# Performance work log

Measured on AMD Instinct MI355X. Metric: run time of the kernel, lower is better.

The kernel has to match this reference:

```python
import jax, jax.numpy as jnp
import numpy as np

N_NODES = 100000
N_EDGES = 3200000
IN_CH, HID, OUT_CH = 128, 16, 64


def gcn_conv(x, W, b, row, col, n_nodes):
    # PyG GCNConv: add self loops, symmetric deg^{-1/2} normalization,
    # linear transform, scatter-add aggregation at target nodes (col).
    x = x @ W  # [N, out]
    deg = jax.ops.segment_sum(jnp.ones_like(col, dtype=x.dtype), col,
                              num_segments=n_nodes)  # includes self loops
    inv_sqrt = jnp.where(deg > 0, jax.lax.rsqrt(deg), 0.0)
    norm = inv_sqrt[row] * inv_sqrt[col]  # [E+N]
    msgs = x[row] * norm[:, None]  # gather + scale
    out = jax.ops.segment_sum(msgs, col, num_segments=n_nodes)
    return out + b


def setup_inputs() -> dict:
    key = jax.random.key(0)
    ks = jax.random.split(key, 12)
    x = jax.random.normal(ks[0], (N_NODES, IN_CH), dtype=jnp.float32)
    edge_index = jax.random.randint(ks[1], (2, N_EDGES), 0, N_NODES, dtype=jnp.int64)

    def glorot(k, fan_in, fan_out):
        s = jnp.sqrt(6.0 / (fan_in + fan_out))
        return jax.random.uniform(k, (fan_in, fan_out), jnp.float32, -s, s)

    return {
        'x': x,
        'edge_index': edge_index,
        'conv1_W': glorot(ks[2], IN_CH, HID),
        'conv1_b': jnp.zeros((HID,), jnp.float32),
        'conv2_W': glorot(ks[3], HID, OUT_CH),
        'conv2_b': jnp.zeros((OUT_CH,), jnp.float32),
        't1_W': glorot(ks[4], IN_CH, HID),
        't1_b': jnp.zeros((HID,), jnp.float32),
        't2_W': glorot(ks[5], HID, OUT_CH),
        't2_b': jnp.zeros((OUT_CH,), jnp.float32),
    }


def reference(x, edge_index, conv1_W, conv1_b, conv2_W, conv2_b,
              t1_W, t1_b, t2_W, t2_b):
    n = x.shape[0]
    # add self loops once (fixed shape)
    loops = jnp.arange(n, dtype=edge_index.dtype)
    row = jnp.concatenate([edge_index[0], loops])
    col = jnp.concatenate([edge_index[1], loops])

    identity1 = x @ t1_W + t1_b
    h = jax.nn.relu(gcn_conv(x, conv1_W, conv1_b, row, col, n)) + identity1
    identity2 = h @ t2_W + t2_b
    out = jax.nn.relu(gcn_conv(h, conv2_W, conv2_b, row, col, n)) + identity2
    return out
```

## Files before the change

### kernel.cpp

```cpp
#include <hip/hip_runtime.h>

#define INCH 128
#define C1   16
#define C2   64
#define LOCB 7
#define BNODES (1 << LOCB)
#define CAP  8192
#define ROWBITS 17
#define ROWMASK ((1 << ROWBITS) - 1)
#define SENT 0xFFFFFFFFu
#define ACC2P 9
#define FXS   512.0f
#define INVFX 0.001953125f
#define U16B  32768.5f
#define BSH   15
#define BKT_T 1024
#define AGG_T 512

typedef int iv4 __attribute__((ext_vector_type(4)));

__global__ void binit_kernel(int* __restrict__ gcur, int K) {
    int t = blockIdx.x * blockDim.x + threadIdx.x;
    if (t < K) gcur[t] = t * CAP;
}

__global__ __launch_bounds__(BKT_T) void bucket_kernel(
    const int* __restrict__ row, const int* __restrict__ col,
    int* __restrict__ gcur, int* __restrict__ barr,
    int e, int n, int K, int nblocks)
{
    __shared__ int cnt[1024];
    __shared__ int cur[1024];
    __shared__ int sst[1024];
    int tid = threadIdx.x;
    int e4 = e >> 2;
    long b0 = (long)blockIdx.x * e4 / nblocks;
    long b1 = (long)(blockIdx.x + 1) * e4 / nblocks;
    const iv4* c4p = (const iv4*)col;
    const iv4* r4p = (const iv4*)row;
    cnt[tid] = 0;
    __syncthreads();
    for (long i = b0 + tid; i < b1; i += BKT_T) {
        iv4 c4 = c4p[i], r4 = r4p[i];
        #pragma unroll
        for (int k = 0; k < 4; ++k) {
            unsigned c = (unsigned)c4[k], r = (unsigned)r4[k];
            if (c < (unsigned)n && r < (unsigned)n)
                atomicAdd(&cnt[c >> LOCB], 1);
        }
    }
    if (blockIdx.x == 0) {
        for (int i = e4 * 4 + tid; i < e; i += BKT_T) {
            unsigned c = (unsigned)col[i], r = (unsigned)row[i];
            if (c < (unsigned)n && r < (unsigned)n)
                atomicAdd(&cnt[c >> LOCB], 1);
        }
    }
    __syncthreads();
    if (tid < K) {
        int c = cnt[tid];
        int start = c ? atomicAdd(&gcur[tid], (c + 15) & ~15) : 0;
        cur[tid] = start;
        sst[tid] = start;
    }
    __syncthreads();
    for (long i = b0 + tid; i < b1; i += BKT_T) {
        iv4 c4 = c4p[i], r4 = r4p[i];
        #pragma unroll
        for (int k = 0; k < 4; ++k) {
            unsigned c = (unsigned)c4[k], r = (unsigned)r4[k];
            if (c < (unsigned)n && r < (unsigned)n) {
                int b = c >> LOCB;
                int slot = atomicAdd(&cur[b], 1);
                if ((unsigned)slot < (unsigned)((b + 1) * CAP))
                    barr[slot] = (int)(r | ((c & (BNODES - 1)) << ROWBITS));
            }
        }
    }
    if (blockIdx.x == 0) {
        for (int i = e4 * 4 + tid; i < e; i += BKT_T) {
            unsigned c = (unsigned)col[i], r = (unsigned)row[i];
            if (c < (unsigned)n && r < (unsigned)n) {
                int b = c >> LOCB;
                int slot = atomicAdd(&cur[b], 1);
                if ((unsigned)slot < (unsigned)((b + 1) * CAP))
                    barr[slot] = (int)(r | ((c & (BNODES - 1)) << ROWBITS));
            }
        }
    }
    __syncthreads();
    if (tid < K) {
        int c = cnt[tid];
        if (c) {
            int start = sst[tid];
            int end = start + c;
            int re  = start + ((c + 15) & ~15);
            int lim = (tid + 1) * CAP;
            if (end > lim) end = lim;
            if (re  > lim) re  = lim;
            for (int j = end; j < re; ++j) barr[j] = (int)SENT;
        }
    }
}

__global__ __launch_bounds__(AGG_T) void degree_kernel(
    const int* __restrict__ barr, const int* __restrict__ gcur,
    int* __restrict__ deg, int n)
{
    __shared__ int lcnt[BNODES];
    int b = blockIdx.x, tid = threadIdx.x;
    if (tid < BNODES) lcnt[tid] = 0;
    __syncthreads();
    int base = b * CAP;
    int len = gcur[b] - base;
    if (len < 0) len = 0;
    if (len > CAP) len = CAP;
    int len4 = len >> 2;
    const iv4* b4 = (const iv4*)(barr + base);
    for (int i = tid; i < len4; i += AGG_T) {
        iv4 p4 = b4[i];
        #pragma unroll
        for (int k = 0; k < 4; ++k) {
            unsigned pk = (unsigned)p4[k];
            if ((pk & ROWMASK) < (unsigned)n)
                atomicAdd(&lcnt[(pk >> ROWBITS) & (BNODES - 1)], 1);
        }
    }
    __syncthreads();
    if (tid < BNODES) {
        int node = (b << LOCB) + tid;
        if (node < n) deg[node] = lcnt[tid];
    }
}

__device__ __forceinline__ unsigned short enc16(float v) {
    float c = fminf(fmaxf(v, -63.0f), 63.0f);
    return (unsigned short)(c * FXS + U16B);
}

__global__ __launch_bounds__(256) void linear1_kernel(
    const float* __restrict__ x, const float* __restrict__ W1,
    const float* __restrict__ T1, const float* __restrict__ t1b,
    const int* __restrict__ deg,
    unsigned short* __restrict__ xu16, float* __restrict__ xT1, int n)
{
    __shared__ float Wc[INCH][32];
    __shared__ float xs[16][INCH + 4];
    int tid = threadIdx.x;

    for (int i = tid; i < INCH * C1; i += 256) {
        int k = i / C1, c = i % C1;
        Wc[k][c]      = W1[i];
        Wc[k][c + 16] = T1[i];
    }
    int node0 = blockIdx.x * 16;
    for (int i = tid; i < 16 * (INCH / 4); i += 256) {
        int r = i / (INCH / 4);
        int cc = i % (INCH / 4);
        int node = node0 + r;
        float4 v = make_float4(0.f, 0.f, 0.f, 0.f);
        if (node < n) v = ((const float4*)x)[(size_t)node * (INCH / 4) + cc];
        ((float4*)&xs[r][0])[cc] = v;
    }
    __syncthreads();

    int ch = tid & 15, nl = tid >> 4;
    int node = node0 + nl;
    if (node >= n) return;
    float a1 = 0.f, a2 = 0.f;
    #pragma unroll
    for (int k = 0; k < INCH; ++k) {
        float xv = xs[nl][k];
        a1 += xv * Wc[k][ch];
        a2 += xv * Wc[k][ch + 16];
    }
    float ic = rsqrtf((float)(deg[node] + 1));
    xu16[(node << 4) + ch] = enc16(a1 * ic);
    xT1[(node << 4) + ch]  = a2 + t1b[ch];
}

#define EDGE_GS(PK, G)                                                        \
    do {                                                                      \
        if (((PK) & ROWMASK) < un) {                                          \
            unsigned long long* _a = &acc[(((PK) >> ROWBITS) & (BNODES - 1))][tb]; \
            _Pragma("unroll")                                                 \
            for (int _j = 0; _j < 4; ++_j) {                                  \
                unsigned _d = (unsigned)(G)[_j];                              \
                atomicAdd(&_a[_j],                                            \
                    ((unsigned long long)(_d >> 16) << 32) | (_d & 0xFFFFu)); \
            }                                                                 \
        }                                                                     \
    } while (0)

#define GATHER_SCATTER(TBL)                                                   \
    {                                                                         \
        int jj = tid >> 1;                                                    \
        for (int i0 = jj * 4; i0 + 3 < len; i0 += (AGG_T * 2)) {              \
            iv4 w = *(const iv4*)(bp + i0);                                   \
            unsigned s0 = (unsigned)w[0] & ROWMASK, s1 = (unsigned)w[1] & ROWMASK; \
            unsigned s2 = (unsigned)w[2] & ROWMASK, s3 = (unsigned)w[3] & ROWMASK; \
            unsigned c0 = s0 < un ? s0 : 0u, c1 = s1 < un ? s1 : 0u;          \
            unsigned c2 = s2 < un ? s2 : 0u, c3 = s3 < un ? s3 : 0u;          \
            iv4 g0 = *(const iv4*)(TBL + ((size_t)c0 << 3) + tb4);            \
            iv4 g1 = *(const iv4*)(TBL + ((size_t)c1 << 3) + tb4);            \
            iv4 g2 = *(const iv4*)(TBL + ((size_t)c2 << 3) + tb4);            \
            iv4 g3 = *(const iv4*)(TBL + ((size_t)c3 << 3) + tb4);            \
            EDGE_GS((unsigned)w[0], g0);                                      \
            EDGE_GS((unsigned)w[1], g1);                                      \
            EDGE_GS((unsigned)w[2], g2);                                      \
            EDGE_GS((unsigned)w[3], g3);                                      \
        }                                                                     \
    }

__global__ __launch_bounds__(AGG_T) void agg1_bucket_kernel(
    const int* __restrict__ barr, const int* __restrict__ gcur,
    const int* __restrict__ deg, const unsigned short* __restrict__ xu16,
    const float* __restrict__ xT1, const float* __restrict__ b1,
    float* __restrict__ h, unsigned short* __restrict__ hu16, int n)
{
    __shared__ unsigned long long acc[BNODES][ACC2P];
    int b = blockIdx.x, tid = threadIdx.x;
    for (int i = tid; i < BNODES * ACC2P; i += AGG_T) (&acc[0][0])[i] = 0ull;
    __syncthreads();

    int base = b * CAP;
    int len = gcur[b] - base;
    if (len < 0) len = 0;
    if (len > CAP) len = CAP;
    const int* bp = barr + base;
    const unsigned* tblw = (const unsigned*)xu16;
    unsigned un = (unsigned)n;
    int tb4 = (tid & 1) << 2;
    int tb  = (tid & 1) << 2;

    GATHER_SCATTER(tblw)
    __syncthreads();

    const unsigned* au = (const unsigned*)&acc[0][0];
    for (int t = tid; t < BNODES * C1; t += AGG_T) {
        int loc = t >> 4, ch = t & 15;
        int node = (b << LOCB) + loc;
        if (node >= n) continue;
        int idx = (node << 4) + ch;
        int dg = deg[node];
        unsigned wd = au[loc * (2 * ACC2P) + ch];
        int tot = (int)(wd + xu16[idx] - ((unsigned)(dg + 1) << BSH));
        float ic = rsqrtf((float)(dg + 1));
        float v = (float)tot * INVFX * ic + b1[ch];
        float hv = fmaxf(v, 0.f) + xT1[idx];
        h[idx]    = hv;
        hu16[idx] = enc16(hv * ic);
    }
}

__global__ __launch_bounds__(AGG_T) void agg2_bucket_kernel(
    const int* __restrict__ barr, const int* __restrict__ gcur,
    const int* __restrict__ deg, const unsigned short* __restrict__ hu16,
    const float* __restrict__ h,
    const float* __restrict__ W2, const float* __restrict__ T2,
    const float* __restrict__ b2, const float* __restrict__ t2b,
    float* __restrict__ out, int n)
{
    __shared__ unsigned long long acc[BNODES][ACC2P];
    __shared__ float Wc[C1][128];
    __shared__ float h_s[BNODES][C1];
    __shared__ float accf[BNODES][C1 + 1];
    int b = blockIdx.x, tid = threadIdx.x;
    for (int i = tid; i < BNODES * ACC2P; i += AGG_T) (&acc[0][0])[i] = 0ull;
    for (int i = tid; i < C1 * 128; i += AGG_T) {
        int k = i >> 7, c = i & 127;
        Wc[k][c] = (c < 64) ? W2[k * C2 + c] : T2[k * C2 + (c - 64)];
    }
    {
        int node0 = b << LOCB;
        for (int t = tid; t < BNODES * C1 / 4; t += AGG_T) {
            float4 v = make_float4(0.f, 0.f, 0.f, 0.f);
            if (node0 + (t >> 2) < n) v = ((const float4*)h)[(size_t)node0 * 4 + t];
            ((float4*)&h_s[0][0])[t] = v;
        }
    }
    __syncthreads();

    int base = b * CAP;
    int len = gcur[b] - base;
    if (len < 0) len = 0;
    if (len > CAP) len = CAP;
    const int* bp = barr + base;
    const unsigned* tblw = (const unsigned*)hu16;
    unsigned un = (unsigned)n;
    int tb4 = (tid & 1) << 2;
    int tb  = (tid & 1) << 2;

    GATHER_SCATTER(tblw)
    __syncthreads();

    const unsigned* au = (const unsigned*)&acc[0][0];
    for (int t = tid; t < BNODES * C1; t += AGG_T) {
        int loc = t >> 4, ch = t & 15;
        int node = (b << LOCB) + loc;
        float v = 0.f;
        if (node < n) {
            int dg = deg[node];
            unsigned wd = au[loc * (2 * ACC2P) + ch];
            int tot = (int)(wd + hu16[(node << 4) + ch] - ((unsigned)(dg + 1) << BSH));
            v = (float)tot * INVFX * rsqrtf((float)(dg + 1));
        }
        accf[loc][ch] = v;
    }
    __syncthreads();

    int och = tid & 63, g = tid >> 6;
    float w1r[C1], w2r[C1];
    #pragma unroll
    for (int k = 0; k < C1; ++k) { w1r[k] = Wc[k][och]; w2r[k] = Wc[k][och + 64]; }
    float bb = b2[och], tb2 = t2b[och];
    for (int q = 0; q < 16; ++q) {
        int loc = (g << 4) + q;
        int node2 = (b << LOCB) + loc;
        if (node2 >= n) continue;
        float s1 = bb, s2 = tb2;
        #pragma unroll
        for (int k = 0; k < C1; ++k) {
            s1 += accf[loc][k] * w1r[k];
            s2 += h_s[loc][k]  * w2r[k];
        }
        out[(size_t)node2 * C2 + och] = fmaxf(s1, 0.f) + s2;
    }
}

extern "C" void kernel_launch(void* const* d_in, const int* in_sizes, int n_in,
                              void* d_out, int out_size, void* d_ws, size_t ws_size,
                              hipStream_t stream) {
    const float* x   = (const float*)d_in[0];
    const int*   ei  = (const int*)d_in[1];
    const float* W1  = (const float*)d_in[2];
    const float* b1  = (const float*)d_in[3];
    const float* W2  = (const float*)d_in[4];
    const float* b2  = (const float*)d_in[5];
    const float* T1  = (const float*)d_in[6];
    const float* t1b = (const float*)d_in[7];
    const float* T2  = (const float*)d_in[8];
    const float* t2b = (const float*)d_in[9];
    float* out = (float*)d_out;

    const int n = in_sizes[0] / INCH;
    const int e = in_sizes[1] / 2;
    const int* row = ei;
    const int* col = ei + e;
    const int K = (n + BNODES - 1) >> LOCB;

    char* ws = (char*)d_ws;
    int*            gcur = (int*)ws;                  ws += 4096;
    int*            deg  = (int*)ws;                  ws += (size_t)n * 4;
    float*          xT1  = (float*)ws;                ws += (size_t)n * C1 * 4;
    float*          h    = (float*)ws;                ws += (size_t)n * C1 * 4;
    unsigned short* xu16 = (unsigned short*)ws;       ws += (size_t)n * C1 * 2;
    unsigned short* hu16 = (unsigned short*)ws;       ws += (size_t)n * C1 * 2;
    int*            barr = (int*)ws;                  ws += (size_t)K * CAP * 4;

    const int nbb = 390;

    binit_kernel  <<<(K + 255) / 256, 256, 0, stream>>>(gcur, K);
    bucket_kernel <<<nbb, BKT_T, 0, stream>>>(row, col, gcur, barr, e, n, K, nbb);
    degree_kernel <<<K, AGG_T, 0, stream>>>(barr, gcur, deg, n);

    linear1_kernel <<<(n + 15) / 16, 256, 0, stream>>>(x, W1, T1, t1b, deg, xu16, xT1, n);
    agg1_bucket_kernel<<<K, AGG_T, 0, stream>>>(barr, gcur, deg, xu16, xT1, b1, h, hu16, n);
    agg2_bucket_kernel<<<K, AGG_T, 0, stream>>>(barr, gcur, deg, hu16, h,
                                                W2, T2, b2, t2b, out, n);
}
```

Baseline: 250.9 us.

## Raise fixed-point scale, replace bucket init with memset, vectorize linear1 dot

Switches the bucket cursor to relative offsets so the init kernel can be replaced by a hipMemsetAsync, and the aggregation kernels compute the base from the bucket index. The linear1 weights are stored transposed so each thread reads float4 vectors from shared memory with four partial sums, instead of scalar strided reads. Separately, the 16-bit fixed-point encoding is changed to scale 1024 with a clamp at ±31. That gains precision but raises the risk of saturating large activations or overflowing accumulators.

```diff
diff --git a/kernel.cpp b/kernel.cpp
--- a/kernel.cpp
+++ b/kernel.cpp
@@ -10,19 +10,14 @@
 #define ROWMASK ((1 << ROWBITS) - 1)
 #define SENT 0xFFFFFFFFu
 #define ACC2P 9
-#define FXS   512.0f
-#define INVFX 0.001953125f
+#define FXS   1024.0f
+#define INVFX 0.0009765625f
 #define U16B  32768.5f
 #define BSH   15
 #define BKT_T 1024
 #define AGG_T 512
 
 typedef int iv4 __attribute__((ext_vector_type(4)));
-
-__global__ void binit_kernel(int* __restrict__ gcur, int K) {
-    int t = blockIdx.x * blockDim.x + threadIdx.x;
-    if (t < K) gcur[t] = t * CAP;
-}
 
 __global__ __launch_bounds__(BKT_T) void bucket_kernel(
     const int* __restrict__ row, const int* __restrict__ col,
@@ -59,7 +54,8 @@
     __syncthreads();
     if (tid < K) {
         int c = cnt[tid];
-        int start = c ? atomicAdd(&gcur[tid], (c + 15) & ~15) : 0;
+        int rel = c ? atomicAdd(&gcur[tid], (c + 15) & ~15) : 0;
+        int start = tid * CAP + rel;
         cur[tid] = start;
         sst[tid] = start;
     }
@@ -111,12 +107,11 @@
     int b = blockIdx.x, tid = threadIdx.x;
     if (tid < BNODES) lcnt[tid] = 0;
     __syncthreads();
-    int base = b * CAP;
-    int len = gcur[b] - base;
+    int len = gcur[b];
     if (len < 0) len = 0;
     if (len > CAP) len = CAP;
     int len4 = len >> 2;
-    const iv4* b4 = (const iv4*)(barr + base);
+    const iv4* b4 = (const iv4*)(barr + b * CAP);
     for (int i = tid; i < len4; i += AGG_T) {
         iv4 p4 = b4[i];
         #pragma unroll
@@ -134,7 +129,7 @@
 }
 
 __device__ __forceinline__ unsigned short enc16(float v) {
-    float c = fminf(fmaxf(v, -63.0f), 63.0f);
+    float c = fminf(fmaxf(v, -31.0f), 31.0f);
     return (unsigned short)(c * FXS + U16B);
 }
 
@@ -144,19 +139,18 @@
     const int* __restrict__ deg,
     unsigned short* __restrict__ xu16, float* __restrict__ xT1, int n)
 {
-    __shared__ float Wc[INCH][32];
+    __shared__ float WcT[32][INCH + 4];
     __shared__ float xs[16][INCH + 4];
     int tid = threadIdx.x;
 
     for (int i = tid; i < INCH * C1; i += 256) {
-        int k = i / C1, c = i % C1;
-        Wc[k][c]      = W1[i];
-        Wc[k][c + 16] = T1[i];
+        int k = i >> 4, c = i & 15;
+        WcT[c][k]      = W1[i];
+        WcT[c + 16][k] = T1[i];
     }
     int node0 = blockIdx.x * 16;
     for (int i = tid; i < 16 * (INCH / 4); i += 256) {
-        int r = i / (INCH / 4);
-        int cc = i % (INCH / 4);
+        int r = i >> 5, cc = i & 31;
         int node = node0 + r;
         float4 v = make_float4(0.f, 0.f, 0.f, 0.f);
         if (node < n) v = ((const float4*)x)[(size_t)node * (INCH / 4) + cc];
@@ -167,13 +161,23 @@
     int ch = tid & 15, nl = tid >> 4;
     int node = node0 + nl;
     if (node >= n) return;
-    float a1 = 0.f, a2 = 0.f;
+    const float4* xp  = (const float4*)&xs[nl][0];
+    const float4* w1p = (const float4*)&WcT[ch][0];
+    const float4* w2p = (const float4*)&WcT[ch + 16][0];
+    float4 s1 = make_float4(0.f, 0.f, 0.f, 0.f);
+    float4 s2 = make_float4(0.f, 0.f, 0.f, 0.f);
     #pragma unroll
-    for (int k = 0; k < INCH; ++k) {
-        float xv = xs[nl][k];
-        a1 += xv * Wc[k][ch];
-        a2 += xv * Wc[k][ch + 16];
-    }
+    for (int k4 = 0; k4 < INCH / 4; ++k4) {
+        float4 xv = xp[k4];
+        float4 wa = w1p[k4];
+        float4 wb = w2p[k4];
+        s1.x += xv.x * wa.x; s1.y += xv.y * wa.y;
+        s1.z += xv.z * wa.z; s1.w += xv.w * wa.w;
+        s2.x += xv.x * wb.x; s2.y += xv.y * wb.y;
+        s2.z += xv.z * wb.z; s2.w += xv.w * wb.w;
+    }
+    float a1 = (s1.x + s1.y) + (s1.z + s1.w);
+    float a2 = (s2.x + s2.y) + (s2.z + s2.w);
     float ic = rsqrtf((float)(deg[node] + 1));
     xu16[(node << 4) + ch] = enc16(a1 * ic);
     xT1[(node << 4) + ch]  = a2 + t1b[ch];
@@ -223,11 +227,10 @@
     for (int i = tid; i < BNODES * ACC2P; i += AGG_T) (&acc[0][0])[i] = 0ull;
     __syncthreads();
 
-    int base = b * CAP;
-    int len = gcur[b] - base;
+    int len = gcur[b];
     if (len < 0) len = 0;
     if (len > CAP) len = CAP;
-    const int* bp = barr + base;
+    const int* bp = barr + b * CAP;
     const unsigned* tblw = (const unsigned*)xu16;
     unsigned un = (unsigned)n;
     int tb4 = (tid & 1) << 2;
@@ -281,11 +284,10 @@
     }
     __syncthreads();
 
-    int base = b * CAP;
-    int len = gcur[b] - base;
+    int len = gcur[b];
     if (len < 0) len = 0;
     if (len > CAP) len = CAP;
-    const int* bp = barr + base;
+    const int* bp = barr + b * CAP;
     const unsigned* tblw = (const unsigned*)hu16;
     unsigned un = (unsigned)n;
     int tb4 = (tid & 1) << 2;
@@ -360,7 +362,7 @@
 
     const int nbb = 390;
 
-    binit_kernel  <<<(K + 255) / 256, 256, 0, stream>>>(gcur, K);
+    hipMemsetAsync(gcur, 0, 4096, stream);
     bucket_kernel <<<nbb, BKT_T, 0, stream>>>(row, col, gcur, barr, e, n, K, nbb);
     degree_kernel <<<K, AGG_T, 0, stream>>>(barr, gcur, deg, n);
 
```

Measured after the change: 250.9 us. About the same (+0.0%).
